# Kernel optimization log

Hardware: AMD Instinct MI355X
Metric: run time of the kernel (lower is better)

The kernel has to match this reference:

```python
import jax, jax.numpy as jnp
import numpy as np

N, IN_FEAT, OUT_FEAT, H = 4096, 256, 256, 8
D = OUT_FEAT // H  # per-head dim = 32
ADJ_DENSITY = 0.05


def setup_inputs() -> dict:
    key = jax.random.key(0)
    kx, kw, kb, ka, kadj = jax.random.split(key, 5)
    x = jax.random.normal(kx, (N, IN_FEAT), dtype=jnp.float32)
    # eqx.nn.Linear params: weight [out, in], bias [out]
    W = jax.random.normal(kw, (OUT_FEAT, IN_FEAT), dtype=jnp.float32) * (1.0 / np.sqrt(IN_FEAT))
    b = jax.random.normal(kb, (OUT_FEAT,), dtype=jnp.float32) * 0.01
    a = jax.random.normal(ka, (H, 2 * D), dtype=jnp.float32)
    adj_matrix = jax.random.bernoulli(kadj, ADJ_DENSITY, (N, N)).astype(jnp.float32)
    return {"x": x, "W": W, "b": b, "a": a, "adj_matrix": adj_matrix}


def reference(x, W, b, a, adj_matrix):
    num_nodes = x.shape[0]
    num_heads = a.shape[0]
    half = a.shape[1] // 2
    # projection: [N, H*D] -> [N, H, D]
    node_feats = (x @ W.T + b).reshape(num_nodes, num_heads, half)
    # per-head additive attention halves -> [N, H]
    logit_parent = (node_feats * a[None, :, :half]).sum(axis=-1)
    logit_child = (node_feats * a[None, :, half:]).sum(axis=-1)
    # [N, N, H] dense logits via broadcast-add
    attn_logits = logit_parent[:, None, :] + logit_child[None, :, :]
    attn_logits = jax.nn.leaky_relu(attn_logits, 0.2)
    # NOTE: faithful to source — masked entries set to 0.0 (not -inf)
    attn_logits = jnp.where(jnp.abs(adj_matrix)[..., None] != 0.0, attn_logits, 0.0)
    attn_probs = jax.nn.softmax(attn_logits, axis=1)
    out = jnp.einsum('ijh,jhc->ihc', attn_probs, node_feats)
    return out.reshape(num_nodes, -1)
```

## Files before the change

### kernel.cpp

```cpp
#include <hip/hip_runtime.h>

#define NN    4096
#define OF    256
#define NH    8
#define MAXNZ 512

typedef __attribute__((ext_vector_type(8))) short short8;
typedef __attribute__((ext_vector_type(4))) float f32x4;

__device__ __forceinline__ float bf2f(unsigned int u) {
    union { unsigned int i; float f; } v; v.i = u << 16; return v.f;
}
__device__ __forceinline__ unsigned short f2bf(float f) {
    union { float f; unsigned int i; } v; v.f = f;
    unsigned int x = v.i;
    return (unsigned short)((x + 0x7fffu + ((x >> 16) & 1u)) >> 16);
}
__device__ __forceinline__ unsigned int pk2bf(float a, float b) {
    return (unsigned int)f2bf(a) | ((unsigned int)f2bf(b) << 16);
}

__global__ __launch_bounds__(256) void k_proj(
    const void* __restrict__ xraw, const void* __restrict__ Wraw,
    const void* __restrict__ braw, const float* __restrict__ adjf,
    float* __restrict__ nf, unsigned short* __restrict__ nfb,
    float* __restrict__ Stot, int* __restrict__ flag)
{
    __shared__ int viol;
    int t = threadIdx.x;
    if (t == 0) viol = 0;
    __syncthreads();
    int bad = 0;
    for (int k = t; k < NN; k += 256) {
        float v = adjf[k];
        if (!(v == 0.0f || v == 1.0f)) bad = 1;
    }
    if (bad) atomicAdd(&viol, 1);
    __syncthreads();
    int f = viol > 0;
    if (t == 0 && blockIdx.x == 0) *flag = f;

    int wave = t >> 6;
    int lane = t & 63;
    int tid  = blockIdx.x * 4 + wave;
    int mt = tid >> 4, nt = tid & 15;
    int lr = lane & 15;
    int kq = (lane >> 4) * 8;

    f32x4 acc = {0.f, 0.f, 0.f, 0.f};
    if (f) {
        const short8* xp = reinterpret_cast<const short8*>(
            (const unsigned short*)xraw + (size_t)(mt*16 + lr)*OF + kq);
        const short8* wp = reinterpret_cast<const short8*>(
            (const unsigned short*)Wraw + (size_t)(nt*16 + lr)*OF + kq);
        #pragma unroll
        for (int kk = 0; kk < OF/32; kk++)
            acc = __builtin_amdgcn_mfma_f32_16x16x32_bf16(xp[kk*4], wp[kk*4], acc, 0, 0, 0);
    } else {
        const float* xp = (const float*)xraw + (size_t)(mt*16 + lr)*OF + kq;
        const float* wp = (const float*)Wraw + (size_t)(nt*16 + lr)*OF + kq;
        #pragma unroll
        for (int kk = 0; kk < OF/32; kk++) {
            short8 ah, al, bh, bl;
            #pragma unroll
            for (int e = 0; e < 8; e++) {
                float xv = xp[kk*32 + e];
                unsigned short h = f2bf(xv);
                ah[e] = (short)h; al[e] = (short)f2bf(xv - bf2f(h));
                float wv = wp[kk*32 + e];
                unsigned short g = f2bf(wv);
                bh[e] = (short)g; bl[e] = (short)f2bf(wv - bf2f(g));
            }
            acc = __builtin_amdgcn_mfma_f32_16x16x32_bf16(ah, bh, acc, 0, 0, 0);
            acc = __builtin_amdgcn_mfma_f32_16x16x32_bf16(ah, bl, acc, 0, 0, 0);
            acc = __builtin_amdgcn_mfma_f32_16x16x32_bf16(al, bh, acc, 0, 0, 0);
        }
    }

    int col  = nt*16 + lr;
    int row0 = mt*16 + (lane >> 4) * 4;
    float bias = f ? bf2f((unsigned int)((const unsigned short*)braw)[col])
                   : ((const float*)braw)[col];
    float csum = 0.f;
    #pragma unroll
    for (int r = 0; r < 4; r++) {
        float v = acc[r] + bias;
        size_t off = (size_t)(row0 + r) * OF + col;
        nf[off]  = v;
        nfb[off] = f2bf(v);
        csum += v;
    }
    csum += __shfl_down(csum, 16, 64);
    csum += __shfl_down(csum, 32, 64);
    if (lane < 16) atomicAdd(&Stot[col], csum);
}

__global__ __launch_bounds__(256) void k_logits(
    const float* __restrict__ nf, const void* __restrict__ asrc,
    const int* __restrict__ flag, float* __restrict__ lp, float* __restrict__ lc)
{
    __shared__ float as[512];
    int f = *flag;
    int t = threadIdx.x;
    for (int s = t; s < 512; s += 256)
        as[s] = f ? bf2f((unsigned int)((const unsigned short*)asrc)[s])
                  : ((const float*)asrc)[s];
    __syncthreads();
    int gid = blockIdx.x * 256 + t;
    int i = gid >> 3, h = gid & 7;
    const float4* row = reinterpret_cast<const float4*>(nf + (size_t)i*OF + h*32);
    const float* ap = as + h * 64;
    float p = 0.f, c = 0.f;
    #pragma unroll
    for (int q = 0; q < 8; q++) {
        float4 v = row[q];
        p += v.x*ap[q*4+0] + v.y*ap[q*4+1] + v.z*ap[q*4+2] + v.w*ap[q*4+3];
        c += v.x*ap[32+q*4+0] + v.y*ap[32+q*4+1] + v.z*ap[32+q*4+2] + v.w*ap[32+q*4+3];
    }
    lp[gid] = p; lc[gid] = c;
}

__global__ __launch_bounds__(256) void k_attn(
    const int* __restrict__ flag, const void* __restrict__ adjv,
    const float* __restrict__ lp, const float* __restrict__ lc,
    const unsigned short* __restrict__ nfb, const float* __restrict__ Stot,
    void* __restrict__ outv)
{
    __shared__ float lps[NH];
    __shared__ int   wsum[4];
    __shared__ int   jro[MAXNZ];
    __shared__ float wlist[MAXNZ][NH];
    __shared__ float zred[256];
    __shared__ float gred[3][256];

    int i = blockIdx.x;
    int t = threadIdx.x;
    int lane = t & 63, wid = t >> 6;
    int f = *flag;
    if (t < NH) lps[t] = lp[i*NH + t];

    unsigned int mask16 = 0;
    if (f) {
        const uint4* arow = reinterpret_cast<const uint4*>(
            (const unsigned short*)adjv + (size_t)i * NN);
        uint4 v0 = arow[t*2], v1 = arow[t*2 + 1];
        unsigned int w[8] = {v0.x, v0.y, v0.z, v0.w, v1.x, v1.y, v1.z, v1.w};
        #pragma unroll
        for (int q = 0; q < 8; q++) {
            if (w[q] & 0xffffu) mask16 |= 1u << (2*q);
            if (w[q] >> 16)     mask16 |= 1u << (2*q + 1);
        }
    } else {
        const uint4* arow = reinterpret_cast<const uint4*>(
            (const float*)adjv + (size_t)i * NN);
        #pragma unroll
        for (int q = 0; q < 4; q++) {
            uint4 v = arow[t*4 + q];
            if (v.x) mask16 |= 1u << (4*q);
            if (v.y) mask16 |= 1u << (4*q + 1);
            if (v.z) mask16 |= 1u << (4*q + 2);
            if (v.w) mask16 |= 1u << (4*q + 3);
        }
    }

    int pc = __popc(mask16);
    int pref = pc;
    #pragma unroll
    for (int off = 1; off < 64; off <<= 1) {
        int u = __shfl_up(pref, off, 64);
        if (lane >= off) pref += u;
    }
    if (lane == 63) wsum[wid] = pref;
    __syncthreads();
    int wb = pref - pc;
    if (wid > 0) wb += wsum[0];
    if (wid > 1) wb += wsum[1];
    if (wid > 2) wb += wsum[2];
    int n = wsum[0] + wsum[1] + wsum[2] + wsum[3];
    n = min(n, MAXNZ);
    {
        int pos = wb, jb = t * 16;
        unsigned int mm = mask16;
        while (mm && pos < MAXNZ) {
            int q = __builtin_ctz(mm);
            mm &= mm - 1;
            jro[pos++] = (jb + q) * OF;
        }
    }
    __syncthreads();

    int h8 = t & 7, c32 = t >> 3;
    float lph = lps[h8];
    float zp = 0.f;
    for (int k = c32; k < n; k += 32) {
        float s = lph + lc[(jro[k] >> 5) + h8];
        s = s > 0.f ? s : 0.2f * s;
        float w = __expf(fminf(s, 70.f)) - 1.f;
        wlist[k][h8] = w;
        zp += w;
    }
    zred[t] = zp;
    __syncthreads();

    int hh = lane >> 3;
    int c4 = lane * 4;
    float a0 = 0.f, a1 = 0.f, a2 = 0.f, a3 = 0.f;
    for (int k = wid; k < n; k += 4) {
        float w = wlist[k][hh];
        uint2 pk = *reinterpret_cast<const uint2*>(nfb + (size_t)(jro[k] + c4));
        a0 += w * bf2f(pk.x & 0xffffu);
        a1 += w * bf2f(pk.x >> 16);
        a2 += w * bf2f(pk.y & 0xffffu);
        a3 += w * bf2f(pk.y >> 16);
    }
    if (wid) {
        gred[wid-1][c4]   = a0; gred[wid-1][c4+1] = a1;
        gred[wid-1][c4+2] = a2; gred[wid-1][c4+3] = a3;
    }
    __syncthreads();

    if (wid == 0) {
        float z = zred[lane] + zred[lane+64] + zred[lane+128] + zred[lane+192];
        z += __shfl_down(z, 32, 64);
        z += __shfl_down(z, 16, 64);
        z += __shfl_down(z, 8, 64);
        float zfull = __shfl(z, hh, 64);
        float iz = 1.0f / (4096.0f + zfull);
        a0 += gred[0][c4]   + gred[1][c4]   + gred[2][c4];
        a1 += gred[0][c4+1] + gred[1][c4+1] + gred[2][c4+1];
        a2 += gred[0][c4+2] + gred[1][c4+2] + gred[2][c4+2];
        a3 += gred[0][c4+3] + gred[1][c4+3] + gred[2][c4+3];
        float4 st = *reinterpret_cast<const float4*>(Stot + c4);
        float o0 = (st.x + a0) * iz;
        float o1 = (st.y + a1) * iz;
        float o2 = (st.z + a2) * iz;
        float o3 = (st.w + a3) * iz;
        if (f) {
            uint2 pk; pk.x = pk2bf(o0, o1); pk.y = pk2bf(o2, o3);
            *reinterpret_cast<uint2*>((unsigned short*)outv + (size_t)i*OF + c4) = pk;
        } else {
            float4 o = {o0, o1, o2, o3};
            *reinterpret_cast<float4*>((float*)outv + (size_t)i*OF + c4) = o;
        }
    }
}

extern "C" void kernel_launch(void* const* d_in, const int* in_sizes, int n_in,
                              void* d_out, int out_size, void* d_ws, size_t ws_size,
                              hipStream_t stream) {
    const void* x   = d_in[0];
    const void* W   = d_in[1];
    const void* b   = d_in[2];
    const void* a   = d_in[3];
    const void* adj = d_in[4];

    char* ws = (char*)d_ws;
    const size_t MB = 1024u*1024u, KB = 1024u;
    float*          nf   = (float*)(ws);
    unsigned short* nfb  = (unsigned short*)(ws + 4*MB);
    float*          lp   = (float*)(ws + 6*MB);
    float*          lc   = (float*)(ws + 6*MB + 128*KB);
    float*          Stot = (float*)(ws + 6*MB + 256*KB);
    int*            flag = (int*)(ws + 6*MB + 257*KB);

    hipMemsetAsync(Stot, 0, OF * sizeof(float), stream);
    k_proj  <<<1024, 256, 0, stream>>>(x, W, b, (const float*)adj, nf, nfb, Stot, flag);
    k_logits<<<128,  256, 0, stream>>>(nf, a, flag, lp, lc);
    k_attn  <<<NN,   256, 0, stream>>>(flag, adj, lp, lc, nfb, Stot, d_out);
}
```

Measured before the change: 175.0 us.

## Fuse attention logit computation into projection epilogue and unroll attention gather loops

Removes the separate logits kernel and the fp32 node-feature buffer. The projection epilogue now multiplies each output by the attention vectors, reduces across the 16 lanes of a head via xor shuffles, and atomically adds into zeroed lp/lc buffers. The attention kernel's weight loop is unrolled by two and its gather-accumulate loop by four, so several independent bf16 row loads are in flight at once. This saves a launch and a 4MB write/read round trip, at the cost of extra shuffles and atomics in the projection kernel and floating-point accumulation order that is no longer fixed.

```diff
diff --git a/kernel.cpp b/kernel.cpp
--- a/kernel.cpp
+++ b/kernel.cpp
@@ -22,9 +22,10 @@
 
 __global__ __launch_bounds__(256) void k_proj(
     const void* __restrict__ xraw, const void* __restrict__ Wraw,
-    const void* __restrict__ braw, const float* __restrict__ adjf,
-    float* __restrict__ nf, unsigned short* __restrict__ nfb,
-    float* __restrict__ Stot, int* __restrict__ flag)
+    const void* __restrict__ braw, const void* __restrict__ araw,
+    const float* __restrict__ adjf,
+    unsigned short* __restrict__ nfb, float* __restrict__ lp,
+    float* __restrict__ lc, float* __restrict__ Stot, int* __restrict__ flag)
 {
     __shared__ int viol;
     int t = threadIdx.x;
@@ -79,45 +80,44 @@
 
     int col  = nt*16 + lr;
     int row0 = mt*16 + (lane >> 4) * 4;
-    float bias = f ? bf2f((unsigned int)((const unsigned short*)braw)[col])
-                   : ((const float*)braw)[col];
-    float csum = 0.f;
+    int h = col >> 5, cc = col & 31;
+    float bias, apar, achd;
+    if (f) {
+        bias = bf2f((unsigned int)((const unsigned short*)braw)[col]);
+        apar = bf2f((unsigned int)((const unsigned short*)araw)[h*64 + cc]);
+        achd = bf2f((unsigned int)((const unsigned short*)araw)[h*64 + 32 + cc]);
+    } else {
+        bias = ((const float*)braw)[col];
+        apar = ((const float*)araw)[h*64 + cc];
+        achd = ((const float*)araw)[h*64 + 32 + cc];
+    }
+    float st = 0.f, pr[4], cr[4];
     #pragma unroll
     for (int r = 0; r < 4; r++) {
         float v = acc[r] + bias;
-        size_t off = (size_t)(row0 + r) * OF + col;
-        nf[off]  = v;
-        nfb[off] = f2bf(v);
-        csum += v;
-    }
-    csum += __shfl_down(csum, 16, 64);
-    csum += __shfl_down(csum, 32, 64);
-    if (lane < 16) atomicAdd(&Stot[col], csum);
-}
-
-__global__ __launch_bounds__(256) void k_logits(
-    const float* __restrict__ nf, const void* __restrict__ asrc,
-    const int* __restrict__ flag, float* __restrict__ lp, float* __restrict__ lc)
-{
-    __shared__ float as[512];
-    int f = *flag;
-    int t = threadIdx.x;
-    for (int s = t; s < 512; s += 256)
-        as[s] = f ? bf2f((unsigned int)((const unsigned short*)asrc)[s])
-                  : ((const float*)asrc)[s];
-    __syncthreads();
-    int gid = blockIdx.x * 256 + t;
-    int i = gid >> 3, h = gid & 7;
-    const float4* row = reinterpret_cast<const float4*>(nf + (size_t)i*OF + h*32);
-    const float* ap = as + h * 64;
-    float p = 0.f, c = 0.f;
+        nfb[(size_t)(row0 + r) * OF + col] = f2bf(v);
+        st += v;
+        pr[r] = v * apar;
+        cr[r] = v * achd;
+    }
     #pragma unroll
-    for (int q = 0; q < 8; q++) {
-        float4 v = row[q];
-        p += v.x*ap[q*4+0] + v.y*ap[q*4+1] + v.z*ap[q*4+2] + v.w*ap[q*4+3];
-        c += v.x*ap[32+q*4+0] + v.y*ap[32+q*4+1] + v.z*ap[32+q*4+2] + v.w*ap[32+q*4+3];
-    }
-    lp[gid] = p; lc[gid] = c;
+    for (int m = 1; m <= 8; m <<= 1) {
+        #pragma unroll
+        for (int r = 0; r < 4; r++) {
+            pr[r] += __shfl_xor(pr[r], m, 64);
+            cr[r] += __shfl_xor(cr[r], m, 64);
+        }
+    }
+    if ((lane & 15) == 0) {
+        #pragma unroll
+        for (int r = 0; r < 4; r++) {
+            atomicAdd(&lp[(row0 + r) * NH + h], pr[r]);
+            atomicAdd(&lc[(row0 + r) * NH + h], cr[r]);
+        }
+    }
+    st += __shfl_down(st, 16, 64);
+    st += __shfl_down(st, 32, 64);
+    if (lane < 16) atomicAdd(&Stot[col], st);
 }
 
 __global__ __launch_bounds__(256) void k_attn(
@@ -192,11 +192,22 @@
     int h8 = t & 7, c32 = t >> 3;
     float lph = lps[h8];
     float zp = 0.f;
-    for (int k = c32; k < n; k += 32) {
-        float s = lph + lc[(jro[k] >> 5) + h8];
+    int k3 = c32;
+    for (; k3 + 32 < n; k3 += 64) {
+        int j0 = jro[k3] >> 5, j1 = jro[k3 + 32] >> 5;
+        float l0 = lc[j0 + h8], l1 = lc[j1 + h8];
+        float s0 = lph + l0; s0 = s0 > 0.f ? s0 : 0.2f * s0;
+        float s1 = lph + l1; s1 = s1 > 0.f ? s1 : 0.2f * s1;
+        float w0 = __expf(fminf(s0, 70.f)) - 1.f;
+        float w1 = __expf(fminf(s1, 70.f)) - 1.f;
+        wlist[k3][h8] = w0; wlist[k3 + 32][h8] = w1;
+        zp += w0 + w1;
+    }
+    if (k3 < n) {
+        float s = lph + lc[(jro[k3] >> 5) + h8];
         s = s > 0.f ? s : 0.2f * s;
         float w = __expf(fminf(s, 70.f)) - 1.f;
-        wlist[k][h8] = w;
+        wlist[k3][h8] = w;
         zp += w;
     }
     zred[t] = zp;
@@ -204,14 +215,33 @@
 
     int hh = lane >> 3;
     int c4 = lane * 4;
+    const unsigned short* nb = nfb + c4;
     float a0 = 0.f, a1 = 0.f, a2 = 0.f, a3 = 0.f;
-    for (int k = wid; k < n; k += 4) {
+    int k = wid;
+    for (; k + 12 < n; k += 16) {
+        int j0 = jro[k], j1 = jro[k+4], j2 = jro[k+8], j3 = jro[k+12];
+        float w0 = wlist[k][hh],   w1 = wlist[k+4][hh];
+        float w2 = wlist[k+8][hh], w3 = wlist[k+12][hh];
+        uint2 d0 = *reinterpret_cast<const uint2*>(nb + j0);
+        uint2 d1 = *reinterpret_cast<const uint2*>(nb + j1);
+        uint2 d2 = *reinterpret_cast<const uint2*>(nb + j2);
+        uint2 d3 = *reinterpret_cast<const uint2*>(nb + j3);
+        a0 += w0*bf2f(d0.x & 0xffffu) + w1*bf2f(d1.x & 0xffffu)
+            + w2*bf2f(d2.x & 0xffffu) + w3*bf2f(d3.x & 0xffffu);
+        a1 += w0*bf2f(d0.x >> 16)     + w1*bf2f(d1.x >> 16)
+            + w2*bf2f(d2.x >> 16)     + w3*bf2f(d3.x >> 16);
+        a2 += w0*bf2f(d0.y & 0xffffu) + w1*bf2f(d1.y & 0xffffu)
+            + w2*bf2f(d2.y & 0xffffu) + w3*bf2f(d3.y & 0xffffu);
+        a3 += w0*bf2f(d0.y >> 16)     + w1*bf2f(d1.y >> 16)
+            + w2*bf2f(d2.y >> 16)     + w3*bf2f(d3.y >> 16);
+    }
+    for (; k < n; k += 4) {
         float w = wlist[k][hh];
-        uint2 pk = *reinterpret_cast<const uint2*>(nfb + (size_t)(jro[k] + c4));
-        a0 += w * bf2f(pk.x & 0xffffu);
-        a1 += w * bf2f(pk.x >> 16);
-        a2 += w * bf2f(pk.y & 0xffffu);
-        a3 += w * bf2f(pk.y >> 16);
+        uint2 d = *reinterpret_cast<const uint2*>(nb + jro[k]);
+        a0 += w * bf2f(d.x & 0xffffu);
+        a1 += w * bf2f(d.x >> 16);
+        a2 += w * bf2f(d.y & 0xffffu);
+        a3 += w * bf2f(d.y >> 16);
     }
     if (wid) {
         gred[wid-1][c4]   = a0; gred[wid-1][c4+1] = a1;
@@ -230,11 +260,11 @@
         a1 += gred[0][c4+1] + gred[1][c4+1] + gred[2][c4+1];
         a2 += gred[0][c4+2] + gred[1][c4+2] + gred[2][c4+2];
         a3 += gred[0][c4+3] + gred[1][c4+3] + gred[2][c4+3];
-        float4 st = *reinterpret_cast<const float4*>(Stot + c4);
-        float o0 = (st.x + a0) * iz;
-        float o1 = (st.y + a1) * iz;
-        float o2 = (st.z + a2) * iz;
-        float o3 = (st.w + a3) * iz;
+        float4 stv = *reinterpret_cast<const float4*>(Stot + c4);
+        float o0 = (stv.x + a0) * iz;
+        float o1 = (stv.y + a1) * iz;
+        float o2 = (stv.z + a2) * iz;
+        float o3 = (stv.w + a3) * iz;
         if (f) {
             uint2 pk; pk.x = pk2bf(o0, o1); pk.y = pk2bf(o2, o3);
             *reinterpret_cast<uint2*>((unsigned short*)outv + (size_t)i*OF + c4) = pk;
@@ -256,15 +286,14 @@
 
     char* ws = (char*)d_ws;
     const size_t MB = 1024u*1024u, KB = 1024u;
-    float*          nf   = (float*)(ws);
-    unsigned short* nfb  = (unsigned short*)(ws + 4*MB);
-    float*          lp   = (float*)(ws + 6*MB);
-    float*          lc   = (float*)(ws + 6*MB + 128*KB);
-    float*          Stot = (float*)(ws + 6*MB + 256*KB);
-    int*            flag = (int*)(ws + 6*MB + 257*KB);
-
-    hipMemsetAsync(Stot, 0, OF * sizeof(float), stream);
-    k_proj  <<<1024, 256, 0, stream>>>(x, W, b, (const float*)adj, nf, nfb, Stot, flag);
-    k_logits<<<128,  256, 0, stream>>>(nf, a, flag, lp, lc);
-    k_attn  <<<NN,   256, 0, stream>>>(flag, adj, lp, lc, nfb, Stot, d_out);
-}
+    unsigned short* nfb  = (unsigned short*)(ws);
+    float*          lp   = (float*)(ws + 2*MB);
+    float*          lc   = (float*)(ws + 2*MB + 128*KB);
+    float*          Stot = (float*)(ws + 2*MB + 256*KB);
+    int*            flag = (int*)(ws + 2*MB + 257*KB);
+
+    hipMemsetAsync(lp, 0, 257*KB, stream);
+    k_proj <<<1024, 256, 0, stream>>>(x, W, b, a, (const float*)adj,
+                                      nfb, lp, lc, Stot, flag);
+    k_attn <<<NN,   256, 0, stream>>>(flag, adj, lp, lc, nfb, Stot, d_out);
+}
```

After: 162.3 us. 1.08x faster.
